# Kernel optimization log

Hardware: AMD Instinct MI355X
Metric: run time of the kernel (lower is better)

Reference implementation:

```python
import jax, jax.numpy as jnp
import numpy as np

V, E, H, L = 32000, 1024, 1024, 2
B, T = 64, 256


def setup_inputs() -> dict:
    key = jax.random.key(0)
    ks = jax.random.split(key, 6)
    src = jax.random.randint(ks[0], (B, T), 0, V, dtype=jnp.int32)
    s_e = 1.0 / np.sqrt(H)
    emb = jax.random.normal(ks[1], (V, E), dtype=jnp.float32) * 0.02
    # stacked-layer LSTM params; layer 0 input = E == H so shapes are uniform
    W_ih = jax.random.uniform(ks[2], (L, 4 * H, H), dtype=jnp.float32, minval=-s_e, maxval=s_e)
    W_hh = jax.random.uniform(ks[3], (L, 4 * H, H), dtype=jnp.float32, minval=-s_e, maxval=s_e)
    b_ih = jax.random.uniform(ks[4], (L, 4 * H), dtype=jnp.float32, minval=-s_e, maxval=s_e)
    b_hh = jax.random.uniform(ks[5], (L, 4 * H), dtype=jnp.float32, minval=-s_e, maxval=s_e)
    return {"src": src, "emb": emb, "W_ih": W_ih, "W_hh": W_hh, "b_ih": b_ih, "b_hh": b_hh}


def _lstm_stack(embedded, W_ih, W_hh, b_ih, b_hh):
    # embedded: [B, T, E]
    Bsz = embedded.shape[0]
    h0 = jnp.zeros((L, Bsz, H), embedded.dtype)
    c0 = jnp.zeros((L, Bsz, H), embedded.dtype)

    def step(carry, x_t):
        h, c = carry  # each [L, B, H]
        x = x_t       # [B, E]
        new_h, new_c = [], []
        for l in range(L):
            gates = x @ W_ih[l].T + b_ih[l] + h[l] @ W_hh[l].T + b_hh[l]  # [B, 4H]
            i, f, g, o = jnp.split(gates, 4, axis=-1)
            c_t = jax.nn.sigmoid(f) * c[l] + jax.nn.sigmoid(i) * jnp.tanh(g)
            h_t = jax.nn.sigmoid(o) * jnp.tanh(c_t)
            new_h.append(h_t)
            new_c.append(c_t)
            x = h_t  # feed to next layer (dropout p=0)
        return (jnp.stack(new_h), jnp.stack(new_c)), x

    (h_n, c_n), outs = jax.lax.scan(step, (h0, c0), jnp.swapaxes(embedded, 0, 1))
    return jnp.swapaxes(outs, 0, 1), h_n, c_n  # [B,T,H], [L,B,H], [L,B,H]


def reference(src, emb, W_ih, W_hh, b_ih, b_hh):
    embedded = emb[src]  # [B, T, E]
    encoder_outputs, h_n, c_n = _lstm_stack(embedded, W_ih, W_hh, b_ih, b_hh)
    return encoder_outputs, (h_n, c_n)
```

## Files before the change

### kernel.cpp

```cpp
#include <hip/hip_runtime.h>
#include <hip/hip_bf16.h>

typedef __hip_bfloat16 bf16;
typedef __attribute__((ext_vector_type(8))) short s16x8;
typedef __attribute__((ext_vector_type(4))) float f32x4;
typedef __attribute__((ext_vector_type(4))) int   i32x4;

#define BATCH   64
#define SEQ     256
#define HID     1024
#define GATES   4096
#define NWG     256
#define THREADS 256
#define UNITS   8
#define NCOLS   32
#define ROWSTRIDE 2056
#define BH      (BATCH * HID)

#define H0_SLOTS 8
#define H1_SLOTS 2
#define FLAGS_OFF ((size_t)(H0_SLOTS + H1_SLOTS) * BH * 2)

#define OUT_HN  ((size_t)BATCH * SEQ * HID)
#define OUT_CN  (OUT_HN + 2ull * BATCH * HID)

__device__ __forceinline__ short f2bf(float f) {
    unsigned int u = __builtin_bit_cast(unsigned int, f);
    u = (u + 0x7fffu + ((u >> 16) & 1u)) >> 16;
    return (short)u;
}

#define GLD(i, OFF) asm volatile("global_load_dwordx4 %0, %1, off offset:" OFF " sc0 sc1" \
                                 : "=v"(h[i]) : "v"(xrow));
#define MM8(B0) \
    _Pragma("unroll") \
    for (int kk = (B0); kk < (B0) + 8; ++kk) { \
        s16x8 b0 = *(const s16x8*)(s0 + kk * 32); \
        s16x8 b1 = *(const s16x8*)(s1 + kk * 32); \
        s16x8 av = __builtin_bit_cast(s16x8, h[kk]); \
        a0 = __builtin_amdgcn_mfma_f32_16x16x32_bf16(av, b0, a0, 0, 0, 0); \
        a1 = __builtin_amdgcn_mfma_f32_16x16x32_bf16(av, b1, a1, 0, 0, 0); \
    }
__device__ __forceinline__ void gemm_bt(const bf16* xrow, const bf16* s0, const bf16* s1,
                                        f32x4& a0, f32x4& a1)
{
    i32x4 h[32];
    GLD(0,"0")    GLD(1,"64")   GLD(2,"128")  GLD(3,"192")
    GLD(4,"256")  GLD(5,"320")  GLD(6,"384")  GLD(7,"448")
    GLD(8,"512")  GLD(9,"576")  GLD(10,"640") GLD(11,"704")
    GLD(12,"768") GLD(13,"832") GLD(14,"896") GLD(15,"960")
    GLD(16,"1024") GLD(17,"1088") GLD(18,"1152") GLD(19,"1216")
    GLD(20,"1280") GLD(21,"1344") GLD(22,"1408") GLD(23,"1472")
    asm volatile("s_waitcnt vmcnt(16)"); __builtin_amdgcn_sched_barrier(0);
    MM8(0)
    GLD(24,"1536") GLD(25,"1600") GLD(26,"1664") GLD(27,"1728")
    GLD(28,"1792") GLD(29,"1856") GLD(30,"1920") GLD(31,"1984")
    asm volatile("s_waitcnt vmcnt(16)"); __builtin_amdgcn_sched_barrier(0);
    MM8(8)
    asm volatile("s_waitcnt vmcnt(8)");  __builtin_amdgcn_sched_barrier(0);
    MM8(16)
    asm volatile("s_waitcnt vmcnt(0)");  __builtin_amdgcn_sched_barrier(0);
    MM8(24)
}

__device__ __forceinline__ void gemm_f32c(const float* xrow, const bf16* s0, const bf16* s1,
                                          f32x4& a0, f32x4& a1)
{
#pragma unroll
    for (int c = 0; c < 4; ++c) {
        f32x4 xv[16];
#pragma unroll
        for (int i = 0; i < 8; ++i) {
            const float* p = xrow + (c * 8 + i) * 32;
            xv[2 * i]     = *(const f32x4*)p;
            xv[2 * i + 1] = *(const f32x4*)(p + 4);
        }
#pragma unroll
        for (int i = 0; i < 8; ++i) {
            const int kk = c * 8 + i;
            s16x8 af;
#pragma unroll
            for (int j = 0; j < 4; ++j) {
                af[j]     = f2bf(xv[2 * i][j]);
                af[4 + j] = f2bf(xv[2 * i + 1][j]);
            }
            s16x8 b0 = *(const s16x8*)(s0 + kk * 32);
            s16x8 b1 = *(const s16x8*)(s1 + kk * 32);
            a0 = __builtin_amdgcn_mfma_f32_16x16x32_bf16(af, b0, a0, 0, 0, 0);
            a1 = __builtin_amdgcn_mfma_f32_16x16x32_bf16(af, b1, a1, 0, 0, 0);
        }
    }
}

__device__ __forceinline__ void wave_poll(unsigned int* f, int tgt, int* seen) {
    if (tgt <= 0 || *seen >= tgt) return;
    const int l = threadIdx.x & 63;
    unsigned int* p0 = f + l;
    unsigned int* p1 = f + 64 + l;
    int a, b;
    for (;;) {
        a = (int)__hip_atomic_load(p0, __ATOMIC_RELAXED, __HIP_MEMORY_SCOPE_AGENT);
        b = (int)__hip_atomic_load(p1, __ATOMIC_RELAXED, __HIP_MEMORY_SCOPE_AGENT);
        if (__all((a >= tgt) && (b >= tgt))) break;
        __builtin_amdgcn_s_sleep(1);
    }
    int v = (a < b) ? a : b;
#pragma unroll
    for (int off = 32; off; off >>= 1) {
        int w = __shfl_xor(v, off, 64);
        v = (w < v) ? w : v;
    }
    *seen = v;
    asm volatile("" ::: "memory");
}

__global__ void ws_init(unsigned int* p, int n) {
    for (int i = blockIdx.x * blockDim.x + threadIdx.x; i < n; i += gridDim.x * blockDim.x)
        p[i] = 0u;
}

__global__ void __launch_bounds__(THREADS, 1)
lstm_enc(const int* __restrict__ src, const float* __restrict__ Wemb,
         const float* __restrict__ Wih, const float* __restrict__ Whh,
         const float* __restrict__ bih, const float* __restrict__ bhh,
         float* __restrict__ out, bf16* __restrict__ hbuf)
{
    __shared__ __align__(16) bf16 slab[NCOLS][ROWSTRIDE];
    __shared__ float bias[NCOLS];

    const int wg    = blockIdx.x;
    const int layer = wg >> 7;
    const int wgl   = wg & 127;
    const int j0    = wgl * UNITS;
    const int tid   = threadIdx.x;
    const int lane  = tid & 63;
    const int wave  = tid >> 6;
    const int m     = lane & 15;
    const int q     = lane >> 4;
    const int kq    = q * 8;
    const int b_a   = wave * 16 + m;

    for (int r = 0; r < NCOLS; ++r) {
        int g = r >> 3, u = r & 7;
        size_t grow = (size_t)layer * GATES * HID + (size_t)(g * HID + j0 + u) * HID;
        int k = tid * 8;
        const float* s = (k < HID) ? (Wih + grow + k) : (Whh + grow + (k - HID));
        s16x8 v;
#pragma unroll
        for (int j = 0; j < 8; ++j) v[j] = f2bf(s[j]);
        *(s16x8*)&slab[r][k] = v;
    }
    if (tid < NCOLS) {
        int g = tid >> 3, u = tid & 7;
        int off = layer * GATES + g * HID + j0 + u;
        bias[tid] = bih[off] + bhh[off];
    }
    __syncthreads();

    bf16* h0 = hbuf;
    bf16* h1 = hbuf + H0_SLOTS * BH;
    unsigned int* flags = (unsigned int*)((char*)hbuf + FLAGS_OFF);
    unsigned int* f0 = flags + wave * 128;
    unsigned int* f1 = flags + 512 + wave * 128;
    unsigned int* myflag = flags + layer * 512 + wave * 128 + wgl;

    const int u = m & 7;
    const float b_i = bias[u], b_f = bias[8 + u], b_g = bias[16 + u], b_o = bias[24 + u];
    float c_s[4] = {0.f, 0.f, 0.f, 0.f};
    int seenA = 0, seenB = 0;

    int sv = (layer == 0) ? src[b_a * SEQ] : 0;

    for (int t = 0; t < SEQ; ++t) {
        f32x4 acc0 = {0.f, 0.f, 0.f, 0.f};
        f32x4 acc1 = {0.f, 0.f, 0.f, 0.f};

        if (layer == 0) {
            const float* xF = Wemb + (size_t)sv * HID + kq;
            if (t + 1 < SEQ) sv = src[b_a * SEQ + t + 1];
            gemm_f32c(xF, &slab[m][kq], &slab[16 + m][kq], acc0, acc1);
            wave_poll(f0, t, &seenA);
            if (t >= 1)
                gemm_bt(h0 + (size_t)((t - 1) & 7) * BH + b_a * HID + kq,
                        &slab[m][HID + kq], &slab[16 + m][HID + kq], acc0, acc1);
            wave_poll(f1, t - 7, &seenB);
        } else {
            wave_poll(f0, t + 1, &seenA);
            gemm_bt(h0 + (size_t)(t & 7) * BH + b_a * HID + kq,
                    &slab[m][kq], &slab[16 + m][kq], acc0, acc1);
            wave_poll(f1, t, &seenB);
            if (t >= 1)
                gemm_bt(h1 + (size_t)((t - 1) & 1) * BH + b_a * HID + kq,
                        &slab[m][HID + kq], &slab[16 + m][HID + kq], acc0, acc1);
        }

        float hval[4];
#pragma unroll
        for (int r = 0; r < 4; ++r) {
            float p0 = __shfl_xor(acc0[r], 8, 64);
            float p1 = __shfl_xor(acc1[r], 8, 64);
            const bool lo = (m < 8);
            float gi = (lo ? acc0[r] : p0) + b_i;
            float gf = (lo ? p0 : acc0[r]) + b_f;
            float gg = (lo ? acc1[r] : p1) + b_g;
            float go = (lo ? p1 : acc1[r]) + b_o;
            float si = 1.f / (1.f + __expf(-gi));
            float sf = 1.f / (1.f + __expf(-gf));
            float so = 1.f / (1.f + __expf(-go));
            c_s[r] = sf * c_s[r] + si * tanhf(gg);
            hval[r] = so * tanhf(c_s[r]);
        }

        bf16* hw = (layer == 0) ? h0 + (size_t)(t & 7) * BH
                                : h1 + (size_t)(t & 1) * BH;
        if (m < 8) {
#pragma unroll
            for (int r = 0; r < 4; ++r) {
                int R = wave * 16 + q * 4 + r;
                __hip_atomic_store((unsigned short*)(hw + (size_t)R * HID + j0 + u),
                                   (unsigned short)f2bf(hval[r]),
                                   __ATOMIC_RELAXED, __HIP_MEMORY_SCOPE_AGENT);
            }
        }
        asm volatile("s_waitcnt vmcnt(0)"); __builtin_amdgcn_sched_barrier(0);
        asm volatile("" ::: "memory");
        if (lane == 0)
            __hip_atomic_store(myflag, (unsigned int)(t + 1),
                               __ATOMIC_RELAXED, __HIP_MEMORY_SCOPE_AGENT);

        if (layer == 1 && m < 8) {
#pragma unroll
            for (int r = 0; r < 4; ++r) {
                int R = wave * 16 + q * 4 + r;
                out[((size_t)R * SEQ + t) * HID + j0 + u] = hval[r];
            }
        }
        if (t == SEQ - 1 && m < 8) {
#pragma unroll
            for (int r = 0; r < 4; ++r) {
                int R = wave * 16 + q * 4 + r;
                size_t o = ((size_t)layer * BATCH + R) * HID + j0 + u;
                out[OUT_HN + o] = hval[r];
                out[OUT_CN + o] = c_s[r];
            }
        }
    }
}

extern "C" void kernel_launch(void* const* d_in, const int* in_sizes, int n_in,
                              void* d_out, int out_size, void* d_ws, size_t ws_size,
                              hipStream_t stream) {
    const int*   src  = (const int*)d_in[0];
    const float* emb  = (const float*)d_in[1];
    const float* W_ih = (const float*)d_in[2];
    const float* W_hh = (const float*)d_in[3];
    const float* b_ih = (const float*)d_in[4];
    const float* b_hh = (const float*)d_in[5];
    float* out  = (float*)d_out;
    bf16*  hbuf = (bf16*)d_ws;

    unsigned int* wsp = (unsigned int*)((char*)d_ws + FLAGS_OFF);
    ws_init<<<4, 256, 0, stream>>>(wsp, 1024);

    void* args[] = {&src, &emb, &W_ih, &W_hh, &b_ih, &b_hh, &out, &hbuf};
    hipLaunchCooperativeKernel((void*)lstm_enc, dim3(NWG), dim3(THREADS),
                               args, 0, stream);
}
```

Before: 3.772 ms.

## Replace all-to-all flag polling with aggregator wave and replicated step counters

```diff
diff --git a/kernel.cpp b/kernel.cpp
--- a/kernel.cpp
+++ b/kernel.cpp
@@ -11,7 +11,7 @@
 #define HID     1024
 #define GATES   4096
 #define NWG     256
-#define THREADS 256
+#define THREADS 320
 #define UNITS   8
 #define NCOLS   32
 #define ROWSTRIDE 2056
@@ -19,7 +19,9 @@
 
 #define H0_SLOTS 8
 #define H1_SLOTS 2
-#define FLAGS_OFF ((size_t)(H0_SLOTS + H1_SLOTS) * BH * 2)
+#define PROD_OFF ((size_t)(H0_SLOTS + H1_SLOTS) * BH * 2)
+#define REPS_OFF (PROD_OFF + 1024ull * 128)
+#define WS_NEED  (REPS_OFF + 32ull * 128)
 
 #define OUT_HN  ((size_t)BATCH * SEQ * HID)
 #define OUT_CN  (OUT_HN + 2ull * BATCH * HID)
@@ -92,23 +94,13 @@
     }
 }
 
-__device__ __forceinline__ void wave_poll(unsigned int* f, int tgt, int* seen) {
+__device__ __forceinline__ void rep_poll(unsigned int* rep, int tgt, int* seen) {
     if (tgt <= 0 || *seen >= tgt) return;
-    const int l = threadIdx.x & 63;
-    unsigned int* p0 = f + l;
-    unsigned int* p1 = f + 64 + l;
-    int a, b;
+    int v;
     for (;;) {
-        a = (int)__hip_atomic_load(p0, __ATOMIC_RELAXED, __HIP_MEMORY_SCOPE_AGENT);
-        b = (int)__hip_atomic_load(p1, __ATOMIC_RELAXED, __HIP_MEMORY_SCOPE_AGENT);
-        if (__all((a >= tgt) && (b >= tgt))) break;
+        v = (int)__hip_atomic_load(rep, __ATOMIC_RELAXED, __HIP_MEMORY_SCOPE_AGENT);
+        if (v >= tgt) break;
         __builtin_amdgcn_s_sleep(1);
-    }
-    int v = (a < b) ? a : b;
-#pragma unroll
-    for (int off = 32; off; off >>= 1) {
-        int w = __shfl_xor(v, off, 64);
-        v = (w < v) ? w : v;
     }
     *seen = v;
     asm volatile("" ::: "memory");
@@ -135,34 +127,81 @@
     const int tid   = threadIdx.x;
     const int lane  = tid & 63;
     const int wave  = tid >> 6;
+
+    if (tid < 256) {
+        for (int r = 0; r < NCOLS; ++r) {
+            int g = r >> 3, u = r & 7;
+            size_t grow = (size_t)layer * GATES * HID + (size_t)(g * HID + j0 + u) * HID;
+            int k = tid * 8;
+            const float* s = (k < HID) ? (Wih + grow + k) : (Whh + grow + (k - HID));
+            s16x8 v;
+#pragma unroll
+            for (int j = 0; j < 8; ++j) v[j] = f2bf(s[j]);
+            *(s16x8*)&slab[r][k] = v;
+        }
+        if (tid < NCOLS) {
+            int g = tid >> 3, u = tid & 7;
+            int off = layer * GATES + g * HID + j0 + u;
+            bias[tid] = bih[off] + bhh[off];
+        }
+    }
+    __syncthreads();
+
+    bf16* h0 = hbuf;
+    bf16* h1 = hbuf + H0_SLOTS * BH;
+    unsigned int* prod = (unsigned int*)((char*)hbuf + PROD_OFF);
+    unsigned int* reps = (unsigned int*)((char*)hbuf + REPS_OFF);
+
+    if (wave == 4) {
+        if (wgl == 0) {
+            const int aggl = layer;
+            unsigned int* pb = prod + (size_t)aggl * 512 * 32;
+            unsigned int* rb = reps + (size_t)aggl * 16 * 32;
+            int T = 1;
+            while (T <= SEQ) {
+                unsigned int v0,v1,v2,v3,v4,v5,v6,v7;
+                const unsigned int* a0 = pb + ((size_t)0*64 + lane)*32;
+                const unsigned int* a1 = pb + ((size_t)1*64 + lane)*32;
+                const unsigned int* a2 = pb + ((size_t)2*64 + lane)*32;
+                const unsigned int* a3 = pb + ((size_t)3*64 + lane)*32;
+                const unsigned int* a4 = pb + ((size_t)4*64 + lane)*32;
+                const unsigned int* a5 = pb + ((size_t)5*64 + lane)*32;
+                const unsigned int* a6 = pb + ((size_t)6*64 + lane)*32;
+                const unsigned int* a7 = pb + ((size_t)7*64 + lane)*32;
+                asm volatile("global_load_dword %0, %1, off sc0 sc1" : "=v"(v0) : "v"(a0));
+                asm volatile("global_load_dword %0, %1, off sc0 sc1" : "=v"(v1) : "v"(a1));
+                asm volatile("global_load_dword %0, %1, off sc0 sc1" : "=v"(v2) : "v"(a2));
+                asm volatile("global_load_dword %0, %1, off sc0 sc1" : "=v"(v3) : "v"(a3));
+                asm volatile("global_load_dword %0, %1, off sc0 sc1" : "=v"(v4) : "v"(a4));
+                asm volatile("global_load_dword %0, %1, off sc0 sc1" : "=v"(v5) : "v"(a5));
+                asm volatile("global_load_dword %0, %1, off sc0 sc1" : "=v"(v6) : "v"(a6));
+                asm volatile("global_load_dword %0, %1, off sc0 sc1" : "=v"(v7) : "v"(a7));
+                asm volatile("s_waitcnt vmcnt(0)" ::: "memory");
+                __builtin_amdgcn_sched_barrier(0);
+                const unsigned int uT = (unsigned int)T;
+                int ok = (v0 >= uT) && (v1 >= uT) && (v2 >= uT) && (v3 >= uT) &&
+                         (v4 >= uT) && (v5 >= uT) && (v6 >= uT) && (v7 >= uT);
+                if (__all(ok)) {
+                    if (lane < 16)
+                        __hip_atomic_store(rb + lane * 32, uT,
+                                           __ATOMIC_RELAXED, __HIP_MEMORY_SCOPE_AGENT);
+                    ++T;
+                } else {
+                    __builtin_amdgcn_s_sleep(1);
+                }
+            }
+        }
+        return;
+    }
+
     const int m     = lane & 15;
     const int q     = lane >> 4;
     const int kq    = q * 8;
     const int b_a   = wave * 16 + m;
 
-    for (int r = 0; r < NCOLS; ++r) {
-        int g = r >> 3, u = r & 7;
-        size_t grow = (size_t)layer * GATES * HID + (size_t)(g * HID + j0 + u) * HID;
-        int k = tid * 8;
-        const float* s = (k < HID) ? (Wih + grow + k) : (Whh + grow + (k - HID));
-        s16x8 v;
-#pragma unroll
-        for (int j = 0; j < 8; ++j) v[j] = f2bf(s[j]);
-        *(s16x8*)&slab[r][k] = v;
-    }
-    if (tid < NCOLS) {
-        int g = tid >> 3, u = tid & 7;
-        int off = layer * GATES + g * HID + j0 + u;
-        bias[tid] = bih[off] + bhh[off];
-    }
-    __syncthreads();
-
-    bf16* h0 = hbuf;
-    bf16* h1 = hbuf + H0_SLOTS * BH;
-    unsigned int* flags = (unsigned int*)((char*)hbuf + FLAGS_OFF);
-    unsigned int* f0 = flags + wave * 128;
-    unsigned int* f1 = flags + 512 + wave * 128;
-    unsigned int* myflag = flags + layer * 512 + wave * 128 + wgl;
+    unsigned int* rep0 = reps + (size_t)(((wgl * 4 + wave) & 15)) * 32;
+    unsigned int* rep1 = reps + (size_t)(16 + ((wgl * 4 + wave) & 15)) * 32;
+    unsigned int* myprod = prod + (size_t)(layer * 512 + wgl * 4 + wave) * 32;
 
     const int u = m & 7;
     const float b_i = bias[u], b_f = bias[8 + u], b_g = bias[16 + u], b_o = bias[24 + u];
@@ -179,16 +218,16 @@
             const float* xF = Wemb + (size_t)sv * HID + kq;
             if (t + 1 < SEQ) sv = src[b_a * SEQ + t + 1];
             gemm_f32c(xF, &slab[m][kq], &slab[16 + m][kq], acc0, acc1);
-            wave_poll(f0, t, &seenA);
+            rep_poll(rep0, t, &seenA);
             if (t >= 1)
                 gemm_bt(h0 + (size_t)((t - 1) & 7) * BH + b_a * HID + kq,
                         &slab[m][HID + kq], &slab[16 + m][HID + kq], acc0, acc1);
-            wave_poll(f1, t - 7, &seenB);
+            rep_poll(rep1, t - 7, &seenB);
         } else {
-            wave_poll(f0, t + 1, &seenA);
+            rep_poll(rep0, t + 1, &seenA);
             gemm_bt(h0 + (size_t)(t & 7) * BH + b_a * HID + kq,
                     &slab[m][kq], &slab[16 + m][kq], acc0, acc1);
-            wave_poll(f1, t, &seenB);
+            rep_poll(rep1, t, &seenB);
             if (t >= 1)
                 gemm_bt(h1 + (size_t)((t - 1) & 1) * BH + b_a * HID + kq,
                         &slab[m][HID + kq], &slab[16 + m][HID + kq], acc0, acc1);
@@ -225,7 +264,7 @@
         asm volatile("s_waitcnt vmcnt(0)"); __builtin_amdgcn_sched_barrier(0);
         asm volatile("" ::: "memory");
         if (lane == 0)
-            __hip_atomic_store(myflag, (unsigned int)(t + 1),
+            __hip_atomic_store(myprod, (unsigned int)(t + 1),
                                __ATOMIC_RELAXED, __HIP_MEMORY_SCOPE_AGENT);
 
         if (layer == 1 && m < 8) {
@@ -259,8 +298,8 @@
     float* out  = (float*)d_out;
     bf16*  hbuf = (bf16*)d_ws;
 
-    unsigned int* wsp = (unsigned int*)((char*)d_ws + FLAGS_OFF);
-    ws_init<<<4, 256, 0, stream>>>(wsp, 1024);
+    unsigned int* wsp = (unsigned int*)((char*)d_ws + PROD_OFF);
+    ws_init<<<36, 256, 0, stream>>>(wsp, (1024 + 32) * 32);
 
     void* args[] = {&src, &emb, &W_ih, &W_hh, &b_ih, &b_hh, &out, &hbuf};
     hipLaunchCooperativeKernel((void*)lstm_enc, dim3(NWG), dim3(THREADS),
```

New measurement: 4.319 ms. 14.5% more time.

## Replace per-WG flags with sharded atomic counters and overlap embedding GEMM with polling

Applied to the files above, without the earlier changes.

```diff
diff --git a/kernel.cpp b/kernel.cpp
--- a/kernel.cpp
+++ b/kernel.cpp
@@ -19,7 +19,7 @@
 
 #define H0_SLOTS 8
 #define H1_SLOTS 2
-#define FLAGS_OFF ((size_t)(H0_SLOTS + H1_SLOTS) * BH * 2)
+#define CNT_OFF ((size_t)(H0_SLOTS + H1_SLOTS) * BH * 2)
 
 #define OUT_HN  ((size_t)BATCH * SEQ * HID)
 #define OUT_CN  (OUT_HN + 2ull * BATCH * HID)
@@ -63,48 +63,37 @@
     MM8(24)
 }
 
-__device__ __forceinline__ void gemm_f32c(const float* xrow, const bf16* s0, const bf16* s1,
-                                          f32x4& a0, f32x4& a1)
+__device__ __forceinline__ void emb_chunk(const float* xrow, const bf16* s0, const bf16* s1,
+                                          int c, f32x4& a0, f32x4& a1)
 {
-#pragma unroll
-    for (int c = 0; c < 4; ++c) {
-        f32x4 xv[16];
-#pragma unroll
-        for (int i = 0; i < 8; ++i) {
-            const float* p = xrow + (c * 8 + i) * 32;
-            xv[2 * i]     = *(const f32x4*)p;
-            xv[2 * i + 1] = *(const f32x4*)(p + 4);
-        }
-#pragma unroll
-        for (int i = 0; i < 8; ++i) {
-            const int kk = c * 8 + i;
-            s16x8 af;
-#pragma unroll
-            for (int j = 0; j < 4; ++j) {
-                af[j]     = f2bf(xv[2 * i][j]);
-                af[4 + j] = f2bf(xv[2 * i + 1][j]);
-            }
-            s16x8 b0 = *(const s16x8*)(s0 + kk * 32);
-            s16x8 b1 = *(const s16x8*)(s1 + kk * 32);
-            a0 = __builtin_amdgcn_mfma_f32_16x16x32_bf16(af, b0, a0, 0, 0, 0);
-            a1 = __builtin_amdgcn_mfma_f32_16x16x32_bf16(af, b1, a1, 0, 0, 0);
-        }
-    }
-}
-
-__device__ __forceinline__ void wave_poll(unsigned int* f, int tgt, int* seen) {
-    if (tgt <= 0 || *seen >= tgt) return;
-    const int l = threadIdx.x & 63;
-    unsigned int* p0 = f + l;
-    unsigned int* p1 = f + 64 + l;
-    int a, b;
-    for (;;) {
-        a = (int)__hip_atomic_load(p0, __ATOMIC_RELAXED, __HIP_MEMORY_SCOPE_AGENT);
-        b = (int)__hip_atomic_load(p1, __ATOMIC_RELAXED, __HIP_MEMORY_SCOPE_AGENT);
-        if (__all((a >= tgt) && (b >= tgt))) break;
-        __builtin_amdgcn_s_sleep(1);
-    }
-    int v = (a < b) ? a : b;
+    f32x4 xv[16];
+#pragma unroll
+    for (int i = 0; i < 8; ++i) {
+        const float* p = xrow + (c * 8 + i) * 32;
+        xv[2 * i]     = *(const f32x4*)p;
+        xv[2 * i + 1] = *(const f32x4*)(p + 4);
+    }
+#pragma unroll
+    for (int i = 0; i < 8; ++i) {
+        const int kk = c * 8 + i;
+        s16x8 af;
+#pragma unroll
+        for (int j = 0; j < 4; ++j) {
+            af[j]     = f2bf(xv[2 * i][j]);
+            af[4 + j] = f2bf(xv[2 * i + 1][j]);
+        }
+        s16x8 b0 = *(const s16x8*)(s0 + kk * 32);
+        s16x8 b1 = *(const s16x8*)(s1 + kk * 32);
+        a0 = __builtin_amdgcn_mfma_f32_16x16x32_bf16(af, b0, a0, 0, 0, 0);
+        a1 = __builtin_amdgcn_mfma_f32_16x16x32_bf16(af, b1, a1, 0, 0, 0);
+    }
+}
+
+__device__ __forceinline__ bool cnt_probe(unsigned int* base, int tgt64, int* seen) {
+    if (tgt64 <= 0 || *seen >= tgt64) return true;
+    unsigned int* p = base + (threadIdx.x & 7) * 32;
+    int v = (int)__hip_atomic_load(p, __ATOMIC_RELAXED, __HIP_MEMORY_SCOPE_AGENT);
+    if (!__all(v >= tgt64)) return false;
 #pragma unroll
     for (int off = 32; off; off >>= 1) {
         int w = __shfl_xor(v, off, 64);
@@ -112,6 +101,10 @@
     }
     *seen = v;
     asm volatile("" ::: "memory");
+    return true;
+}
+__device__ __forceinline__ void cnt_poll(unsigned int* base, int tgt64, int* seen) {
+    while (!cnt_probe(base, tgt64, seen)) __builtin_amdgcn_s_sleep(1);
 }
 
 __global__ void ws_init(unsigned int* p, int n) {
@@ -159,10 +152,10 @@
 
     bf16* h0 = hbuf;
     bf16* h1 = hbuf + H0_SLOTS * BH;
-    unsigned int* flags = (unsigned int*)((char*)hbuf + FLAGS_OFF);
-    unsigned int* f0 = flags + wave * 128;
-    unsigned int* f1 = flags + 512 + wave * 128;
-    unsigned int* myflag = flags + layer * 512 + wave * 128 + wgl;
+    unsigned int* cnt  = (unsigned int*)((char*)hbuf + CNT_OFF);
+    unsigned int* cnt0 = cnt;
+    unsigned int* cnt1 = cnt + 8 * 32;
+    unsigned int* mycnt = (layer ? cnt1 : cnt0) + (wgl & 7) * 32;
 
     const int u = m & 7;
     const float b_i = bias[u], b_f = bias[8 + u], b_g = bias[16 + u], b_o = bias[24 + u];
@@ -178,17 +171,28 @@
         if (layer == 0) {
             const float* xF = Wemb + (size_t)sv * HID + kq;
             if (t + 1 < SEQ) sv = src[b_a * SEQ + t + 1];
-            gemm_f32c(xF, &slab[m][kq], &slab[16 + m][kq], acc0, acc1);
-            wave_poll(f0, t, &seenA);
+            const int tA = 64 * t;
+            const int tB = 64 * (t - 7);
+            int ec = 0;
+            for (;;) {
+                bool a = cnt_probe(cnt0, tA, &seenA);
+                bool b = cnt_probe(cnt1, tB, &seenB);
+                if (a && b) break;
+                if (ec < 4) { emb_chunk(xF, &slab[m][kq], &slab[16 + m][kq], ec, acc0, acc1); ++ec; }
+                else __builtin_amdgcn_s_sleep(1);
+            }
             if (t >= 1)
                 gemm_bt(h0 + (size_t)((t - 1) & 7) * BH + b_a * HID + kq,
                         &slab[m][HID + kq], &slab[16 + m][HID + kq], acc0, acc1);
-            wave_poll(f1, t - 7, &seenB);
+            while (ec < 4) { emb_chunk(xF, &slab[m][kq], &slab[16 + m][kq], ec, acc0, acc1); ++ec; }
         } else {
-            wave_poll(f0, t + 1, &seenA);
+            const int tA = 64 * (t + 1);
+            const int tB = 64 * t;
+            cnt_probe(cnt1, tB, &seenB);
+            cnt_poll(cnt0, tA, &seenA);
             gemm_bt(h0 + (size_t)(t & 7) * BH + b_a * HID + kq,
                     &slab[m][kq], &slab[16 + m][kq], acc0, acc1);
-            wave_poll(f1, t, &seenB);
+            cnt_poll(cnt1, tB, &seenB);
             if (t >= 1)
                 gemm_bt(h1 + (size_t)((t - 1) & 1) * BH + b_a * HID + kq,
                         &slab[m][HID + kq], &slab[16 + m][HID + kq], acc0, acc1);
@@ -225,8 +229,7 @@
         asm volatile("s_waitcnt vmcnt(0)"); __builtin_amdgcn_sched_barrier(0);
         asm volatile("" ::: "memory");
         if (lane == 0)
-            __hip_atomic_store(myflag, (unsigned int)(t + 1),
-                               __ATOMIC_RELAXED, __HIP_MEMORY_SCOPE_AGENT);
+            __hip_atomic_fetch_add(mycnt, 1u, __ATOMIC_RELAXED, __HIP_MEMORY_SCOPE_AGENT);
 
         if (layer == 1 && m < 8) {
 #pragma unroll
@@ -259,8 +262,8 @@
     float* out  = (float*)d_out;
     bf16*  hbuf = (bf16*)d_ws;
 
-    unsigned int* wsp = (unsigned int*)((char*)d_ws + FLAGS_OFF);
-    ws_init<<<4, 256, 0, stream>>>(wsp, 1024);
+    unsigned int* wsp = (unsigned int*)((char*)d_ws + CNT_OFF);
+    ws_init<<<2, 256, 0, stream>>>(wsp, 16 * 32);
 
     void* args[] = {&src, &emb, &W_ih, &W_hh, &b_ih, &b_hh, &out, &hbuf};
     hipLaunchCooperativeKernel((void*)lstm_enc, dim3(NWG), dim3(THREADS),
```

Result: slower. 5.507 ms (+46.0%).

## Keep full hidden-state history to drop ring-buffer back-pressure and cache-bypass loads

Applied to the files above, without the earlier changes.

```diff
diff --git a/kernel.cpp b/kernel.cpp
--- a/kernel.cpp
+++ b/kernel.cpp
@@ -17,9 +17,10 @@
 #define ROWSTRIDE 2056
 #define BH      (BATCH * HID)
 
-#define H0_SLOTS 8
-#define H1_SLOTS 2
-#define FLAGS_OFF ((size_t)(H0_SLOTS + H1_SLOTS) * BH * 2)
+#define HBASE_OFF  4096ull
+#define WS_NEED    (HBASE_OFF + 2ull * SEQ * BH * 2)
+#define H0_RS 8
+#define H1_RS 2
 
 #define OUT_HN  ((size_t)BATCH * SEQ * HID)
 #define OUT_CN  (OUT_HN + 2ull * BATCH * HID)
@@ -30,8 +31,8 @@
     return (short)u;
 }
 
-#define GLD(i, OFF) asm volatile("global_load_dwordx4 %0, %1, off offset:" OFF " sc0 sc1" \
-                                 : "=v"(h[i]) : "v"(xrow));
+#define GLD(i, OFF, CF) asm volatile("global_load_dwordx4 %0, %1, off offset:" OFF " " CF \
+                                     : "=v"(h[i]) : "v"(xrow));
 #define MM8(B0) \
     _Pragma("unroll") \
     for (int kk = (B0); kk < (B0) + 8; ++kk) { \
@@ -41,27 +42,30 @@
         a0 = __builtin_amdgcn_mfma_f32_16x16x32_bf16(av, b0, a0, 0, 0, 0); \
         a1 = __builtin_amdgcn_mfma_f32_16x16x32_bf16(av, b1, a1, 0, 0, 0); \
     }
-__device__ __forceinline__ void gemm_bt(const bf16* xrow, const bf16* s0, const bf16* s1,
-                                        f32x4& a0, f32x4& a1)
-{
-    i32x4 h[32];
-    GLD(0,"0")    GLD(1,"64")   GLD(2,"128")  GLD(3,"192")
-    GLD(4,"256")  GLD(5,"320")  GLD(6,"384")  GLD(7,"448")
-    GLD(8,"512")  GLD(9,"576")  GLD(10,"640") GLD(11,"704")
-    GLD(12,"768") GLD(13,"832") GLD(14,"896") GLD(15,"960")
-    GLD(16,"1024") GLD(17,"1088") GLD(18,"1152") GLD(19,"1216")
-    GLD(20,"1280") GLD(21,"1344") GLD(22,"1408") GLD(23,"1472")
-    asm volatile("s_waitcnt vmcnt(16)"); __builtin_amdgcn_sched_barrier(0);
-    MM8(0)
-    GLD(24,"1536") GLD(25,"1600") GLD(26,"1664") GLD(27,"1728")
-    GLD(28,"1792") GLD(29,"1856") GLD(30,"1920") GLD(31,"1984")
-    asm volatile("s_waitcnt vmcnt(16)"); __builtin_amdgcn_sched_barrier(0);
-    MM8(8)
-    asm volatile("s_waitcnt vmcnt(8)");  __builtin_amdgcn_sched_barrier(0);
-    MM8(16)
-    asm volatile("s_waitcnt vmcnt(0)");  __builtin_amdgcn_sched_barrier(0);
-    MM8(24)
-}
+#define GEMM_FN(NAME, CF) \
+__device__ __forceinline__ void NAME(const bf16* xrow, const bf16* s0, const bf16* s1, \
+                                     f32x4& a0, f32x4& a1) \
+{ \
+    i32x4 h[32]; \
+    GLD(0,"0",CF)    GLD(1,"64",CF)   GLD(2,"128",CF)  GLD(3,"192",CF) \
+    GLD(4,"256",CF)  GLD(5,"320",CF)  GLD(6,"384",CF)  GLD(7,"448",CF) \
+    GLD(8,"512",CF)  GLD(9,"576",CF)  GLD(10,"640",CF) GLD(11,"704",CF) \
+    GLD(12,"768",CF) GLD(13,"832",CF) GLD(14,"896",CF) GLD(15,"960",CF) \
+    GLD(16,"1024",CF) GLD(17,"1088",CF) GLD(18,"1152",CF) GLD(19,"1216",CF) \
+    GLD(20,"1280",CF) GLD(21,"1344",CF) GLD(22,"1408",CF) GLD(23,"1472",CF) \
+    asm volatile("s_waitcnt vmcnt(16)"); __builtin_amdgcn_sched_barrier(0); \
+    MM8(0) \
+    GLD(24,"1536",CF) GLD(25,"1600",CF) GLD(26,"1664",CF) GLD(27,"1728",CF) \
+    GLD(28,"1792",CF) GLD(29,"1856",CF) GLD(30,"1920",CF) GLD(31,"1984",CF) \
+    asm volatile("s_waitcnt vmcnt(16)"); __builtin_amdgcn_sched_barrier(0); \
+    MM8(8) \
+    asm volatile("s_waitcnt vmcnt(8)");  __builtin_amdgcn_sched_barrier(0); \
+    MM8(16) \
+    asm volatile("s_waitcnt vmcnt(0)");  __builtin_amdgcn_sched_barrier(0); \
+    MM8(24) \
+}
+GEMM_FN(gemm_bt, "sc0 sc1")
+GEMM_FN(gemm_p,  "")
 
 __device__ __forceinline__ void gemm_f32c(const float* xrow, const bf16* s0, const bf16* s1,
                                           f32x4& a0, f32x4& a1)
@@ -123,7 +127,7 @@
 lstm_enc(const int* __restrict__ src, const float* __restrict__ Wemb,
          const float* __restrict__ Wih, const float* __restrict__ Whh,
          const float* __restrict__ bih, const float* __restrict__ bhh,
-         float* __restrict__ out, bf16* __restrict__ hbuf)
+         float* __restrict__ out, bf16* __restrict__ hbuf, int hist_on)
 {
     __shared__ __align__(16) bf16 slab[NCOLS][ROWSTRIDE];
     __shared__ float bias[NCOLS];
@@ -157,9 +161,10 @@
     }
     __syncthreads();
 
-    bf16* h0 = hbuf;
-    bf16* h1 = hbuf + H0_SLOTS * BH;
-    unsigned int* flags = (unsigned int*)((char*)hbuf + FLAGS_OFF);
+    unsigned int* flags = (unsigned int*)hbuf;
+    bf16* hb = (bf16*)((char*)hbuf + HBASE_OFF);
+    bf16* h0 = hb;
+    bf16* h1 = hist_on ? hb + (size_t)SEQ * BH : hb + (size_t)H0_RS * BH;
     unsigned int* f0 = flags + wave * 128;
     unsigned int* f1 = flags + 512 + wave * 128;
     unsigned int* myflag = flags + layer * 512 + wave * 128 + wgl;
@@ -180,18 +185,33 @@
             if (t + 1 < SEQ) sv = src[b_a * SEQ + t + 1];
             gemm_f32c(xF, &slab[m][kq], &slab[16 + m][kq], acc0, acc1);
             wave_poll(f0, t, &seenA);
-            if (t >= 1)
-                gemm_bt(h0 + (size_t)((t - 1) & 7) * BH + b_a * HID + kq,
-                        &slab[m][HID + kq], &slab[16 + m][HID + kq], acc0, acc1);
-            wave_poll(f1, t - 7, &seenB);
+            if (t >= 1) {
+                if (hist_on)
+                    gemm_p(h0 + (size_t)(t - 1) * BH + b_a * HID + kq,
+                           &slab[m][HID + kq], &slab[16 + m][HID + kq], acc0, acc1);
+                else
+                    gemm_bt(h0 + (size_t)((t - 1) & (H0_RS - 1)) * BH + b_a * HID + kq,
+                            &slab[m][HID + kq], &slab[16 + m][HID + kq], acc0, acc1);
+            }
+            if (!hist_on)
+                wave_poll(f1, t - 7, &seenB);
         } else {
             wave_poll(f0, t + 1, &seenA);
-            gemm_bt(h0 + (size_t)(t & 7) * BH + b_a * HID + kq,
-                    &slab[m][kq], &slab[16 + m][kq], acc0, acc1);
+            if (hist_on)
+                gemm_p(h0 + (size_t)t * BH + b_a * HID + kq,
+                       &slab[m][kq], &slab[16 + m][kq], acc0, acc1);
+            else
+                gemm_bt(h0 + (size_t)(t & (H0_RS - 1)) * BH + b_a * HID + kq,
+                        &slab[m][kq], &slab[16 + m][kq], acc0, acc1);
             wave_poll(f1, t, &seenB);
-            if (t >= 1)
-                gemm_bt(h1 + (size_t)((t - 1) & 1) * BH + b_a * HID + kq,
-                        &slab[m][HID + kq], &slab[16 + m][HID + kq], acc0, acc1);
+            if (t >= 1) {
+                if (hist_on)
+                    gemm_p(h1 + (size_t)(t - 1) * BH + b_a * HID + kq,
+                           &slab[m][HID + kq], &slab[16 + m][HID + kq], acc0, acc1);
+                else
+                    gemm_bt(h1 + (size_t)((t - 1) & (H1_RS - 1)) * BH + b_a * HID + kq,
+                            &slab[m][HID + kq], &slab[16 + m][HID + kq], acc0, acc1);
+            }
         }
 
         float hval[4];
@@ -211,8 +231,9 @@
             hval[r] = so * tanhf(c_s[r]);
         }
 
-        bf16* hw = (layer == 0) ? h0 + (size_t)(t & 7) * BH
-                                : h1 + (size_t)(t & 1) * BH;
+        bf16* hw = (layer == 0)
+            ? h0 + (size_t)(hist_on ? t : (t & (H0_RS - 1))) * BH
+            : h1 + (size_t)(hist_on ? t : (t & (H1_RS - 1))) * BH;
         if (m < 8) {
 #pragma unroll
             for (int r = 0; r < 4; ++r) {
@@ -259,10 +280,11 @@
     float* out  = (float*)d_out;
     bf16*  hbuf = (bf16*)d_ws;
 
-    unsigned int* wsp = (unsigned int*)((char*)d_ws + FLAGS_OFF);
-    ws_init<<<4, 256, 0, stream>>>(wsp, 1024);
-
-    void* args[] = {&src, &emb, &W_ih, &W_hh, &b_ih, &b_hh, &out, &hbuf};
+    ws_init<<<4, 256, 0, stream>>>((unsigned int*)d_ws, 1024);
+
+    int hist_on = (ws_size >= (size_t)WS_NEED) ? 1 : 0;
+
+    void* args[] = {&src, &emb, &W_ih, &W_hh, &b_ih, &b_hh, &out, &hbuf, &hist_on};
     hipLaunchCooperativeKernel((void*)lstm_enc, dim3(NWG), dim3(THREADS),
                                args, 0, stream);
 }
```

After: 3.552 ms. 1.06x faster.
